# Performance work log

Measured on AMD Instinct MI355X. Metric: run time of the kernel, lower is better.

The kernel has to match this reference:

```python
import jax, jax.numpy as jnp
import numpy as np

N = 8192       # number of nodes (dense NxN attention)
F_IN = 256     # input feature dim
F_OUT = 64     # projected feature dim (F_prime)
NEG_SLOPE = 0.01  # nn.LeakyReLU default


def setup_inputs() -> dict:
    key = jax.random.key(0)
    k0, k1, k2, k3 = jax.random.split(key, 4)
    H = jax.random.normal(k0, (N, F_IN), dtype=jnp.float32)
    # dense 0/1 adjacency; force self-loops so every row has a nonzero denominator
    A = jax.random.randint(k1, (N, N), 0, 2, dtype=jnp.int32)
    A = jnp.maximum(A, jnp.eye(N, dtype=jnp.int32))
    # learned params: W : F_IN -> F_OUT (self.W), a : 2*F_OUT -> 1 (self.a)
    W = jax.random.normal(k2, (F_IN, F_OUT), dtype=jnp.float32) / np.sqrt(F_IN)
    bW = jnp.zeros((F_OUT,), dtype=jnp.float32)
    a_w = jax.random.normal(k3, (2 * F_OUT,), dtype=jnp.float32) / np.sqrt(2 * F_OUT)
    a_b = jnp.zeros((), dtype=jnp.float32)
    return {"H": H, "A": A, "W": W, "bW": bW, "a_w": a_w, "a_b": a_b}


def reference(H, A, W, bW, a_w, a_b):
    # Wh[i] = W(H[i])  -> [N, F_OUT]
    Wh = H @ W + bW
    # a([Wh_i ; Wh_j]) = a1.Wh_i + a2.Wh_j + a_b : decompose the concat-linear
    s_src = Wh @ a_w[:F_OUT]           # [N]
    s_tar = Wh @ a_w[F_OUT:]           # [N]
    logits = s_src[:, None] + s_tar[None, :] + a_b   # [N, N]
    # e_ij = exp(leaky_relu(logits))
    e = jnp.exp(jnp.where(logits >= 0, logits, NEG_SLOPE * logits))
    # denominator masks by adjacency (sum_j e_ij * A_ij), as in the original
    denom = jnp.sum(e * A.astype(e.dtype), axis=1, keepdims=True)  # [N, 1]
    alpha = e / denom                   # NOTE: numerator NOT masked (faithful)
    # H'_i = sigmoid(alpha_i @ Wh)
    return jax.nn.sigmoid(alpha @ Wh)   # [N, F_OUT]
```

## Files before the change

kernel.cpp:

```cpp
#include <hip/hip_runtime.h>

#define NN 8192
#define FIN 256
#define FOUT 64
#define NRANK 256
#define NBLK 1024
#define NUNITS 1024

typedef int iv4 __attribute__((ext_vector_type(4)));

__global__ __launch_bounds__(256) void k1_proj(
    const float* __restrict__ H, const float* __restrict__ W,
    const float* __restrict__ bW, const float* __restrict__ aw,
    const float* __restrict__ ab,
    float* __restrict__ Wh, float* __restrict__ s_src, float* __restrict__ t_tar,
    float* __restrict__ E1, float* __restrict__ E2, float* __restrict__ PP,
    unsigned* __restrict__ ctrs)
{
    __shared__ float Hs[16 * FIN];
    int tid = threadIdx.x;
    if (blockIdx.x == 0 && tid < 4) ctrs[tid] = 0u;
    int i0 = blockIdx.x * 16;
    const float4* Hv = (const float4*)(H + (size_t)i0 * FIN);
    float4* Hsv = (float4*)Hs;
    for (int idx = tid; idx < 16 * FIN / 4; idx += 256) Hsv[idx] = Hv[idx];
    __syncthreads();
    int f = tid & 63, sub = tid >> 6;
    float a1f = aw[f], a2f = aw[64 + f];
    float b = bW[f];
    float acc0 = b, acc1 = b, acc2 = b, acc3 = b;
    const float4* h0v = (const float4*)(Hs + (sub     ) * FIN);
    const float4* h1v = (const float4*)(Hs + (sub +  4) * FIN);
    const float4* h2v = (const float4*)(Hs + (sub +  8) * FIN);
    const float4* h3v = (const float4*)(Hs + (sub + 12) * FIN);
    #pragma unroll 4
    for (int k4 = 0; k4 < FIN / 4; ++k4) {
        float4 h0 = h0v[k4], h1 = h1v[k4], h2 = h2v[k4], h3 = h3v[k4];
        float w0 = W[(4 * k4 + 0) * FOUT + f];
        float w1 = W[(4 * k4 + 1) * FOUT + f];
        float w2 = W[(4 * k4 + 2) * FOUT + f];
        float w3 = W[(4 * k4 + 3) * FOUT + f];
        acc0 += h0.x * w0 + h0.y * w1 + h0.z * w2 + h0.w * w3;
        acc1 += h1.x * w0 + h1.y * w1 + h1.z * w2 + h1.w * w3;
        acc2 += h2.x * w0 + h2.y * w1 + h2.z * w2 + h2.w * w3;
        acc3 += h3.x * w0 + h3.y * w1 + h3.z * w2 + h3.w * w3;
    }
    float accs[4] = {acc0, acc1, acc2, acc3};
    #pragma unroll
    for (int q = 0; q < 4; ++q) {
        int i = i0 + sub + 4 * q;
        float a = accs[q];
        Wh[(size_t)i * FOUT + f] = a;
        float v1 = a * a1f, v2 = a * a2f;
        #pragma unroll
        for (int o = 32; o > 0; o >>= 1) {
            v1 += __shfl_xor(v1, o);
            v2 += __shfl_xor(v2, o);
        }
        if (f == 0) {
            float s = v1 + ab[0];
            float t = v2;
            s_src[i] = s; t_tar[i] = t;
            E1[i] = __expf(s); E2[i] = __expf(0.01f * s);
            PP[2 * i]     = __expf(t);
            PP[2 * i + 1] = __expf(0.01f * t);
        }
    }
}

__global__ __launch_bounds__(256, 4) void kA_rank_denom(
    const int* __restrict__ A,
    const float* __restrict__ t_tar, const float* __restrict__ s_src,
    const float* __restrict__ PP,
    const float* __restrict__ E1, const float* __restrict__ E2,
    int* __restrict__ sorted_idx, int* __restrict__ kidx,
    float* __restrict__ denom, unsigned* __restrict__ ctrs)
{
    __shared__ float Ts[NN];
    __shared__ float red[4][8][2];
    __shared__ unsigned ucur;
    int tid = threadIdx.x, wv = tid >> 6, lane = tid & 63;
    int b = blockIdx.x;

    if (b < NRANK) {
        const float4* tv = (const float4*)t_tar;
        float4* Tsv = (float4*)Ts;
        for (int idx = tid; idx < NN / 4; idx += 256) Tsv[idx] = tv[idx];
        __syncthreads();
        int g0 = b * 32 + wv * 8;
        float tj[8], thr[8];
        int rk[8], kc[8];
        #pragma unroll
        for (int q = 0; q < 8; ++q) {
            tj[q] = Ts[g0 + q];
            thr[q] = -s_src[g0 + q];
            rk[q] = 0; kc[q] = 0;
        }
        for (int k = lane; k < NN; k += 64) {
            float tk = Ts[k];
            #pragma unroll
            for (int q = 0; q < 8; ++q) {
                rk[q] += (tk < tj[q] || (tk == tj[q] && k < g0 + q)) ? 1 : 0;
                kc[q] += (tk < thr[q]) ? 1 : 0;
            }
        }
        #pragma unroll
        for (int q = 0; q < 8; ++q) {
            #pragma unroll
            for (int o = 32; o > 0; o >>= 1) {
                rk[q] += __shfl_xor(rk[q], o);
                kc[q] += __shfl_xor(kc[q], o);
            }
        }
        if (lane == 0) {
            #pragma unroll
            for (int q = 0; q < 8; ++q) {
                sorted_idx[rk[q]] = g0 + q;
                kidx[g0 + q] = kc[q];
            }
        }
    }

    for (;;) {
        if (tid == 0) ucur = atomicAdd(&ctrs[0], 1u);
        __syncthreads();
        unsigned u = ucur;
        __syncthreads();
        if (u >= NUNITS) break;
        int i0 = (int)u * 8;
        float e1r[8], accA[8], accB[8];
        #pragma unroll
        for (int r = 0; r < 8; ++r) { e1r[r] = E1[i0 + r]; accA[r] = 0.f; accB[r] = 0.f; }
        const float4* PPv = (const float4*)PP;
        for (int jv = tid; jv < NN / 4; jv += 256) {
            float4 ppA = PPv[2 * jv];
            float4 ppB = PPv[2 * jv + 1];
            #pragma unroll
            for (int r = 0; r < 8; ++r) {
                const iv4 a4 = __builtin_nontemporal_load(
                    (const iv4*)(A + (size_t)(i0 + r) * NN + jv * 4));
                float e1 = e1r[r];
                {
                    bool c = e1 * ppA.x >= 1.0f;
                    float af = (float)a4.x;
                    accA[r] += af * (c ? ppA.x : 0.0f);
                    accB[r] += af * (c ? 0.0f : ppA.y);
                }
                {
                    bool c = e1 * ppA.z >= 1.0f;
                    float af = (float)a4.y;
                    accA[r] += af * (c ? ppA.z : 0.0f);
                    accB[r] += af * (c ? 0.0f : ppA.w);
                }
                {
                    bool c = e1 * ppB.x >= 1.0f;
                    float af = (float)a4.z;
                    accA[r] += af * (c ? ppB.x : 0.0f);
                    accB[r] += af * (c ? 0.0f : ppB.y);
                }
                {
                    bool c = e1 * ppB.z >= 1.0f;
                    float af = (float)a4.w;
                    accA[r] += af * (c ? ppB.z : 0.0f);
                    accB[r] += af * (c ? 0.0f : ppB.w);
                }
            }
        }
        #pragma unroll
        for (int r = 0; r < 8; ++r) {
            #pragma unroll
            for (int o = 32; o > 0; o >>= 1) {
                accA[r] += __shfl_xor(accA[r], o);
                accB[r] += __shfl_xor(accB[r], o);
            }
        }
        if ((tid & 63) == 0) {
            #pragma unroll
            for (int r = 0; r < 8; ++r) { red[wv][r][0] = accA[r]; red[wv][r][1] = accB[r]; }
        }
        __syncthreads();
        if (tid < 8) {
            float sA = red[0][tid][0] + red[1][tid][0] + red[2][tid][0] + red[3][tid][0];
            float sB = red[0][tid][1] + red[1][tid][1] + red[2][tid][1] + red[3][tid][1];
            denom[i0 + tid] = E1[i0 + tid] * sA + E2[i0 + tid] * sB;
        }
        __syncthreads();
    }
}

__global__ __launch_bounds__(64) void k3a_tots(
    const float* __restrict__ Wh, const float* __restrict__ PP,
    const int* __restrict__ sorted_idx,
    float* __restrict__ tots1, float* __restrict__ tots2)
{
    int c = blockIdx.x, f = threadIdx.x;
    float t1 = 0.f, t2 = 0.f;
    int m0 = c * 32;
    #pragma unroll 8
    for (int m = m0; m < m0 + 32; ++m) {
        int sj = sorted_idx[m];
        float wh = Wh[(size_t)sj * 64 + f];
        t1 += PP[2 * sj]     * wh;
        t2 += PP[2 * sj + 1] * wh;
    }
    tots1[c * 64 + f] = t1; tots2[c * 64 + f] = t2;
}

__global__ __launch_bounds__(64) void k3bc_emit(
    const float* __restrict__ Wh, const float* __restrict__ PP,
    const int* __restrict__ sorted_idx,
    const float* __restrict__ tots1, const float* __restrict__ tots2,
    float* __restrict__ pre2, float* __restrict__ suf1)
{
    int c = blockIdx.x, f = threadIdx.x;
    float o2 = 0.f;
    #pragma unroll 8
    for (int w = 0; w < c; ++w) o2 += tots2[w * 64 + f];
    float o1 = 0.f;
    #pragma unroll 8
    for (int w = c + 1; w < 256; ++w) o1 += tots1[w * 64 + f];
    int m0 = c * 32;
    float whr[32], p1r[32], p2r[32];
    #pragma unroll
    for (int q = 0; q < 32; ++q) {
        int sj = sorted_idx[m0 + q];
        whr[q] = Wh[(size_t)sj * 64 + f];
        p1r[q] = PP[2 * sj]; p2r[q] = PP[2 * sj + 1];
    }
    float run2 = o2;
    #pragma unroll
    for (int q = 0; q < 32; ++q) {
        pre2[(size_t)(m0 + q) * 64 + f] = run2;
        run2 += p2r[q] * whr[q];
    }
    if (c == 255) pre2[(size_t)NN * 64 + f] = run2;
    float run1 = o1;
    #pragma unroll
    for (int q = 31; q >= 0; --q) {
        run1 += p1r[q] * whr[q];
        suf1[(size_t)(m0 + q) * 64 + f] = run1;
    }
    if (c == 255) suf1[(size_t)NN * 64 + f] = 0.f;
}

__global__ __launch_bounds__(256) void k5_out(
    const float* __restrict__ suf1, const float* __restrict__ pre2,
    const int* __restrict__ kidx, const float* __restrict__ E1,
    const float* __restrict__ E2, const float* __restrict__ denom,
    float* __restrict__ out)
{
    int tid = threadIdx.x;
    int f = tid & 63, sub = tid >> 6;
    int i = blockIdx.x * 4 + sub;
    int k = kidx[i];
    float num = E1[i] * suf1[(size_t)k * 64 + f] + E2[i] * pre2[(size_t)k * 64 + f];
    float x = num / denom[i];
    out[(size_t)i * 64 + f] = 1.0f / (1.0f + __expf(-x));
}

extern "C" void kernel_launch(void* const* d_in, const int* in_sizes, int n_in,
                              void* d_out, int out_size, void* d_ws, size_t ws_size,
                              hipStream_t stream) {
    const float* H  = (const float*)d_in[0];
    const int*   A  = (const int*)d_in[1];
    const float* W  = (const float*)d_in[2];
    const float* bW = (const float*)d_in[3];
    const float* aw = (const float*)d_in[4];
    const float* ab = (const float*)d_in[5];
    float* out = (float*)d_out;

    float* ws    = (float*)d_ws;
    float* Wh    = ws;
    float* s_src = Wh + 524288;
    float* t_tar = s_src + 8192;
    float* E1    = t_tar + 8192;
    float* E2    = E1 + 8192;
    float* PP    = E2 + 8192;
    float* pre2  = PP + 16384;
    float* suf1  = pre2 + 524352;
    float* tots1 = suf1 + 524352;
    float* tots2 = tots1 + 16384;
    float* denom = tots2 + 16384;
    int* sorted_idx = (int*)(denom + 8192);
    int* kidx       = sorted_idx + 8192;
    unsigned* ctrs  = (unsigned*)(kidx + 8192);

    hipLaunchKernelGGL(k1_proj, dim3(512), dim3(256), 0, stream,
                       H, W, bW, aw, ab, Wh, s_src, t_tar, E1, E2, PP, ctrs);
    hipLaunchKernelGGL(kA_rank_denom, dim3(NBLK), dim3(256), 0, stream,
                       A, t_tar, s_src, PP, E1, E2, sorted_idx, kidx, denom, ctrs);
    hipLaunchKernelGGL(k3a_tots, dim3(256), dim3(64), 0, stream,
                       Wh, PP, sorted_idx, tots1, tots2);
    hipLaunchKernelGGL(k3bc_emit, dim3(256), dim3(64), 0, stream,
                       Wh, PP, sorted_idx, tots1, tots2, pre2, suf1);
    hipLaunchKernelGGL(k5_out, dim3(2048), dim3(256), 0, stream,
                       suf1, pre2, kidx, E1, E2, denom, out);
}
```

Before: 412.7 us.

## Fold attention vectors into W and move projection GEMM into denominator kernel

The first kernel now computes s_src and t_tar directly as H·(W·a1) and H·(W·a2), precomputing the folded vectors, so it no longer performs the full H@W projection. The Wh GEMM is moved into the big adjacency kernel, where 512 blocks run it alongside the rank blocks before joining the atomic work queue over A rows. This lets the GEMM overlap with the bandwidth-bound A streaming. The denominator work units are halved to 4 rows each with a fully unrolled column loop, which gives finer load balance but uses a different summation order.

```diff
diff --git a/kernel.cpp b/kernel.cpp
--- a/kernel.cpp
+++ b/kernel.cpp
@@ -3,63 +3,69 @@
 #define NN 8192
 #define FIN 256
 #define FOUT 64
+#define NBLK 1024
+#define NGEMM 512
 #define NRANK 256
-#define NBLK 1024
-#define NUNITS 1024
+#define NUNITS 2048
 
 typedef int iv4 __attribute__((ext_vector_type(4)));
 
-__global__ __launch_bounds__(256) void k1_proj(
+__global__ __launch_bounds__(256) void k0_st(
     const float* __restrict__ H, const float* __restrict__ W,
     const float* __restrict__ bW, const float* __restrict__ aw,
     const float* __restrict__ ab,
-    float* __restrict__ Wh, float* __restrict__ s_src, float* __restrict__ t_tar,
+    float* __restrict__ s_src, float* __restrict__ t_tar,
     float* __restrict__ E1, float* __restrict__ E2, float* __restrict__ PP,
     unsigned* __restrict__ ctrs)
 {
-    __shared__ float Hs[16 * FIN];
+    __shared__ float wv1[FIN], wv2[FIN];
     int tid = threadIdx.x;
     if (blockIdx.x == 0 && tid < 4) ctrs[tid] = 0u;
+    {
+        float acc1 = 0.f, acc2 = 0.f;
+        const float4* Wr = (const float4*)(W + (size_t)tid * FOUT);
+        const float4* A1 = (const float4*)aw;
+        const float4* A2 = (const float4*)(aw + FOUT);
+        #pragma unroll
+        for (int f4 = 0; f4 < FOUT / 4; ++f4) {
+            float4 w = Wr[f4], a1 = A1[f4], a2 = A2[f4];
+            acc1 += w.x * a1.x + w.y * a1.y + w.z * a1.z + w.w * a1.w;
+            acc2 += w.x * a2.x + w.y * a2.y + w.z * a2.z + w.w * a2.w;
+        }
+        wv1[tid] = acc1; wv2[tid] = acc2;
+    }
+    float b1 = 0.f, b2 = 0.f;
+    {
+        const float4* Bv = (const float4*)bW;
+        const float4* A1 = (const float4*)aw;
+        const float4* A2 = (const float4*)(aw + FOUT);
+        #pragma unroll
+        for (int f4 = 0; f4 < FOUT / 4; ++f4) {
+            float4 w = Bv[f4], a1 = A1[f4], a2 = A2[f4];
+            b1 += w.x * a1.x + w.y * a1.y + w.z * a1.z + w.w * a1.w;
+            b2 += w.x * a2.x + w.y * a2.y + w.z * a2.z + w.w * a2.w;
+        }
+    }
+    __syncthreads();
+    int wv = tid >> 6, lane = tid & 63;
     int i0 = blockIdx.x * 16;
-    const float4* Hv = (const float4*)(H + (size_t)i0 * FIN);
-    float4* Hsv = (float4*)Hs;
-    for (int idx = tid; idx < 16 * FIN / 4; idx += 256) Hsv[idx] = Hv[idx];
-    __syncthreads();
-    int f = tid & 63, sub = tid >> 6;
-    float a1f = aw[f], a2f = aw[64 + f];
-    float b = bW[f];
-    float acc0 = b, acc1 = b, acc2 = b, acc3 = b;
-    const float4* h0v = (const float4*)(Hs + (sub     ) * FIN);
-    const float4* h1v = (const float4*)(Hs + (sub +  4) * FIN);
-    const float4* h2v = (const float4*)(Hs + (sub +  8) * FIN);
-    const float4* h3v = (const float4*)(Hs + (sub + 12) * FIN);
-    #pragma unroll 4
-    for (int k4 = 0; k4 < FIN / 4; ++k4) {
-        float4 h0 = h0v[k4], h1 = h1v[k4], h2 = h2v[k4], h3 = h3v[k4];
-        float w0 = W[(4 * k4 + 0) * FOUT + f];
-        float w1 = W[(4 * k4 + 1) * FOUT + f];
-        float w2 = W[(4 * k4 + 2) * FOUT + f];
-        float w3 = W[(4 * k4 + 3) * FOUT + f];
-        acc0 += h0.x * w0 + h0.y * w1 + h0.z * w2 + h0.w * w3;
-        acc1 += h1.x * w0 + h1.y * w1 + h1.z * w2 + h1.w * w3;
-        acc2 += h2.x * w0 + h2.y * w1 + h2.z * w2 + h2.w * w3;
-        acc3 += h3.x * w0 + h3.y * w1 + h3.z * w2 + h3.w * w3;
-    }
-    float accs[4] = {acc0, acc1, acc2, acc3};
+    const float4* wv1v = (const float4*)wv1;
+    const float4* wv2v = (const float4*)wv2;
+    float4 v1 = wv1v[lane], v2 = wv2v[lane];
     #pragma unroll
-    for (int q = 0; q < 4; ++q) {
-        int i = i0 + sub + 4 * q;
-        float a = accs[q];
-        Wh[(size_t)i * FOUT + f] = a;
-        float v1 = a * a1f, v2 = a * a2f;
+    for (int r = 0; r < 4; ++r) {
+        int i = i0 + wv * 4 + r;
+        float4 h = ((const float4*)(H + (size_t)i * FIN))[lane];
+        float p1 = h.x * v1.x + h.y * v1.y + h.z * v1.z + h.w * v1.w;
+        float p2 = h.x * v2.x + h.y * v2.y + h.z * v2.z + h.w * v2.w;
         #pragma unroll
         for (int o = 32; o > 0; o >>= 1) {
-            v1 += __shfl_xor(v1, o);
-            v2 += __shfl_xor(v2, o);
-        }
-        if (f == 0) {
-            float s = v1 + ab[0];
-            float t = v2;
+            p1 += __shfl_xor(p1, o);
+            p2 += __shfl_xor(p2, o);
+        }
+        if (lane == 0) {
+            float s = p1 + b1 + ab[0];
+            float t = p2 + b2;
             s_src[i] = s; t_tar[i] = t;
             E1[i] = __expf(s); E2[i] = __expf(0.01f * s);
             PP[2 * i]     = __expf(t);
@@ -68,26 +74,60 @@
     }
 }
 
-__global__ __launch_bounds__(256, 4) void kA_rank_denom(
+__global__ __launch_bounds__(256, 4) void kB_gemm_rank_denom(
     const int* __restrict__ A,
+    const float* __restrict__ H, const float* __restrict__ W,
+    const float* __restrict__ bW,
     const float* __restrict__ t_tar, const float* __restrict__ s_src,
     const float* __restrict__ PP,
     const float* __restrict__ E1, const float* __restrict__ E2,
+    float* __restrict__ Wh,
     int* __restrict__ sorted_idx, int* __restrict__ kidx,
     float* __restrict__ denom, unsigned* __restrict__ ctrs)
 {
     __shared__ float Ts[NN];
-    __shared__ float red[4][8][2];
+    __shared__ float red[4][4][2];
     __shared__ unsigned ucur;
     int tid = threadIdx.x, wv = tid >> 6, lane = tid & 63;
     int b = blockIdx.x;
 
-    if (b < NRANK) {
+    if (b < NGEMM) {
+        float* Hs = Ts;
+        int i0 = b * 16;
+        const float4* Hv = (const float4*)(H + (size_t)i0 * FIN);
+        float4* Hsv = (float4*)Hs;
+        for (int idx = tid; idx < 16 * FIN / 4; idx += 256) Hsv[idx] = Hv[idx];
+        __syncthreads();
+        int f = lane, sub = wv;
+        float bb = bW[f];
+        float acc0 = bb, acc1 = bb, acc2 = bb, acc3 = bb;
+        const float4* h0v = (const float4*)(Hs + (sub     ) * FIN);
+        const float4* h1v = (const float4*)(Hs + (sub +  4) * FIN);
+        const float4* h2v = (const float4*)(Hs + (sub +  8) * FIN);
+        const float4* h3v = (const float4*)(Hs + (sub + 12) * FIN);
+        #pragma unroll 4
+        for (int k4 = 0; k4 < FIN / 4; ++k4) {
+            float4 h0 = h0v[k4], h1 = h1v[k4], h2 = h2v[k4], h3 = h3v[k4];
+            float w0 = W[(4 * k4 + 0) * FOUT + f];
+            float w1 = W[(4 * k4 + 1) * FOUT + f];
+            float w2 = W[(4 * k4 + 2) * FOUT + f];
+            float w3 = W[(4 * k4 + 3) * FOUT + f];
+            acc0 += h0.x * w0 + h0.y * w1 + h0.z * w2 + h0.w * w3;
+            acc1 += h1.x * w0 + h1.y * w1 + h1.z * w2 + h1.w * w3;
+            acc2 += h2.x * w0 + h2.y * w1 + h2.z * w2 + h2.w * w3;
+            acc3 += h3.x * w0 + h3.y * w1 + h3.z * w2 + h3.w * w3;
+        }
+        Wh[(size_t)(i0 + sub     ) * FOUT + f] = acc0;
+        Wh[(size_t)(i0 + sub +  4) * FOUT + f] = acc1;
+        Wh[(size_t)(i0 + sub +  8) * FOUT + f] = acc2;
+        Wh[(size_t)(i0 + sub + 12) * FOUT + f] = acc3;
+        __syncthreads();
+    } else if (b < NGEMM + NRANK) {
         const float4* tv = (const float4*)t_tar;
         float4* Tsv = (float4*)Ts;
         for (int idx = tid; idx < NN / 4; idx += 256) Tsv[idx] = tv[idx];
         __syncthreads();
-        int g0 = b * 32 + wv * 8;
+        int g0 = (b - NGEMM) * 32 + wv * 8;
         float tj[8], thr[8];
         int rk[8], kc[8];
         #pragma unroll
@@ -119,6 +159,7 @@
                 kidx[g0 + q] = kc[q];
             }
         }
+        __syncthreads();
     }
 
     for (;;) {
@@ -127,16 +168,18 @@
         unsigned u = ucur;
         __syncthreads();
         if (u >= NUNITS) break;
-        int i0 = (int)u * 8;
-        float e1r[8], accA[8], accB[8];
-        #pragma unroll
-        for (int r = 0; r < 8; ++r) { e1r[r] = E1[i0 + r]; accA[r] = 0.f; accB[r] = 0.f; }
+        int i0 = (int)u * 4;
+        float e1r[4], accA[4], accB[4];
+        #pragma unroll
+        for (int r = 0; r < 4; ++r) { e1r[r] = E1[i0 + r]; accA[r] = 0.f; accB[r] = 0.f; }
         const float4* PPv = (const float4*)PP;
-        for (int jv = tid; jv < NN / 4; jv += 256) {
+        #pragma unroll
+        for (int m = 0; m < 8; ++m) {
+            int jv = tid + 256 * m;
             float4 ppA = PPv[2 * jv];
             float4 ppB = PPv[2 * jv + 1];
             #pragma unroll
-            for (int r = 0; r < 8; ++r) {
+            for (int r = 0; r < 4; ++r) {
                 const iv4 a4 = __builtin_nontemporal_load(
                     (const iv4*)(A + (size_t)(i0 + r) * NN + jv * 4));
                 float e1 = e1r[r];
@@ -167,7 +210,7 @@
             }
         }
         #pragma unroll
-        for (int r = 0; r < 8; ++r) {
+        for (int r = 0; r < 4; ++r) {
             #pragma unroll
             for (int o = 32; o > 0; o >>= 1) {
                 accA[r] += __shfl_xor(accA[r], o);
@@ -176,10 +219,10 @@
         }
         if ((tid & 63) == 0) {
             #pragma unroll
-            for (int r = 0; r < 8; ++r) { red[wv][r][0] = accA[r]; red[wv][r][1] = accB[r]; }
-        }
-        __syncthreads();
-        if (tid < 8) {
+            for (int r = 0; r < 4; ++r) { red[wv][r][0] = accA[r]; red[wv][r][1] = accB[r]; }
+        }
+        __syncthreads();
+        if (tid < 4) {
             float sA = red[0][tid][0] + red[1][tid][0] + red[2][tid][0] + red[3][tid][0];
             float sB = red[0][tid][1] + red[1][tid][1] + red[2][tid][1] + red[3][tid][1];
             denom[i0 + tid] = E1[i0 + tid] * sA + E2[i0 + tid] * sB;
@@ -285,10 +328,11 @@
     int* kidx       = sorted_idx + 8192;
     unsigned* ctrs  = (unsigned*)(kidx + 8192);
 
-    hipLaunchKernelGGL(k1_proj, dim3(512), dim3(256), 0, stream,
-                       H, W, bW, aw, ab, Wh, s_src, t_tar, E1, E2, PP, ctrs);
-    hipLaunchKernelGGL(kA_rank_denom, dim3(NBLK), dim3(256), 0, stream,
-                       A, t_tar, s_src, PP, E1, E2, sorted_idx, kidx, denom, ctrs);
+    hipLaunchKernelGGL(k0_st, dim3(512), dim3(256), 0, stream,
+                       H, W, bW, aw, ab, s_src, t_tar, E1, E2, PP, ctrs);
+    hipLaunchKernelGGL(kB_gemm_rank_denom, dim3(NBLK), dim3(256), 0, stream,
+                       A, H, W, bW, t_tar, s_src, PP, E1, E2,
+                       Wh, sorted_idx, kidx, denom, ctrs);
     hipLaunchKernelGGL(k3a_tots, dim3(256), dim3(64), 0, stream,
                        Wh, PP, sorted_idx, tots1, tots2);
     hipLaunchKernelGGL(k3bc_emit, dim3(256), dim3(64), 0, stream,
```

After: 397.3 us. 1.04x faster.
